# Kernel optimization log

Measured on AMD Instinct MI355X. Metric: run time of the kernel, lower is better.

## Reference

```python
import jax, jax.numpy as jnp
import numpy as np


def squash(s):
    # s: (..., d); v = ||s|| / (1 + ||s||^2) * s
    norm = jnp.linalg.norm(s, axis=-1, keepdims=True)
    return norm / (1.0 + norm * norm) * s


def setup_inputs() -> dict:
    key = jax.random.key(0)
    k1, k2, k3 = jax.random.split(key, 3)
    batch, n_in, d_in, n_out, d_out = 256, 1152, 8, 10, 16
    u_i = jax.random.normal(k1, (batch, n_in, d_in), dtype=jnp.float32)
    weight = jax.random.normal(k2, (1, n_in, n_out, d_in, d_out), dtype=jnp.float32)
    bias = jax.random.normal(k3, (n_in, n_out, 1), dtype=jnp.float32)
    return {"u_i": u_i, "weight": weight, "bias": bias, "r": 3}


def reference(u_i, weight, bias, r):
    batch, n_in, d_in = u_i.shape
    # predictions u_j|i: (batch, n_in, n_out, d_out)
    u_ji = jnp.einsum('bnd,node->bnoe', u_i, weight[0]) + bias  # bias (n_in,n_out,1) broadcasts over d_out
    # dynamic routing
    b = jnp.zeros(u_ji.shape[:3], dtype=u_ji.dtype)  # (batch, n_in, n_out)
    v = None
    for _ in range(r):  # r is a small static iteration count
        c = jax.nn.softmax(b, axis=-1)                      # over n_out
        s = jnp.einsum('bno,bnoe->boe', c, u_ji)            # weighted sum over n_in
        v = squash(s)                                       # (batch, n_out, d_out)
        b = b + jnp.einsum('bnoe,boe->bno', u_ji, v)        # agreement update
    return v
```

## Files before the change

### kernel.cpp

```cpp
#include <hip/hip_runtime.h>


#define B    256
#define N    1152
#define NO   10
#define DI   8
#define DE   16
#define NTILE   8
#define NTILES  144
#define BG      64
#define BGS     4
#define THREADS 320
#define KT      (NTILE * DI)

#define SP_OFF 0
#define SP_SZ  (NTILES * B * NO * DE)
#define VS_OFF (SP_OFF + SP_SZ)
#define VS_SZ  (B * NO * DE)

__global__ __launch_bounds__(THREADS, 3)
void routing_kernel(const float* __restrict__ u,
                    const float* __restrict__ w,
                    const float* __restrict__ bias,
                    const float* __restrict__ vsum,
                    float* __restrict__ s_part,
                    const int has_v) {
    __shared__ float lds_u[KT * BG];
    __shared__ float lgx[2][NO][BG];
    const int tid  = threadIdx.x;
    const int lane = tid & 63;
    const int wv   = __builtin_amdgcn_readfirstlane(tid >> 6);
    const int o0   = wv * 2;
    const int b0   = blockIdx.y * BG;
    const int b    = b0 + lane;
    const int n0   = blockIdx.x * NTILE;

    for (int i = tid; i < BG * (KT / 4); i += THREADS) {
        const int r  = i >> 4;
        const int c4 = i & 15;
        const float4 v4 = *((const float4*)u + (size_t)(b0 + r) * (N * DI / 4)
                            + n0 * (DI / 4) + c4);
        const int k = c4 * 4;
        lds_u[(k + 0) * BG + r] = v4.x;
        lds_u[(k + 1) * BG + r] = v4.y;
        lds_u[(k + 2) * BG + r] = v4.z;
        lds_u[(k + 3) * BG + r] = v4.w;
    }

    float4 vv[2][4];
#pragma unroll
    for (int oi = 0; oi < 2; ++oi)
#pragma unroll
        for (int eq = 0; eq < 4; ++eq)
            vv[oi][eq] = make_float4(0.f, 0.f, 0.f, 0.f);
    if (has_v) {
#pragma unroll
        for (int oi = 0; oi < 2; ++oi)
#pragma unroll
            for (int eq = 0; eq < 4; ++eq)
                vv[oi][eq] = *(const float4*)(vsum + ((size_t)b * NO + o0 + oi) * DE + eq * 4);
    }

    float4 acc[2][4];
#pragma unroll
    for (int oi = 0; oi < 2; ++oi)
#pragma unroll
        for (int eq = 0; eq < 4; ++eq)
            acc[oi][eq] = make_float4(0.f, 0.f, 0.f, 0.f);

    __syncthreads();

    for (int i = 0; i < NTILE; ++i) {
        const int n = n0 + i;

        float ur[DI];
#pragma unroll
        for (int d = 0; d < DI; ++d) ur[d] = lds_u[(i * DI + d) * BG + lane];

        const float* wp = w + ((size_t)n * NO + o0) * (DI * DE);
        float4 uji[2][4];
#pragma unroll
        for (int oi = 0; oi < 2; ++oi) {
            const float bv = bias[n * NO + o0 + oi];
#pragma unroll
            for (int eq = 0; eq < 4; ++eq)
                uji[oi][eq] = make_float4(bv, bv, bv, bv);
#pragma unroll
            for (int d = 0; d < DI; ++d) {
                const float* wrow = wp + oi * (DI * DE) + d * DE;
#pragma unroll
                for (int eq = 0; eq < 4; ++eq) {
                    const float4 w4 = *(const float4*)(wrow + eq * 4);
                    uji[oi][eq].x += ur[d] * w4.x;
                    uji[oi][eq].y += ur[d] * w4.y;
                    uji[oi][eq].z += ur[d] * w4.z;
                    uji[oi][eq].w += ur[d] * w4.w;
                }
            }
        }

        float c[2];
        if (has_v) {
            const int buf = i & 1;
#pragma unroll
            for (int oi = 0; oi < 2; ++oi) {
                float lg = 0.f;
#pragma unroll
                for (int eq = 0; eq < 4; ++eq)
                    lg += uji[oi][eq].x * vv[oi][eq].x + uji[oi][eq].y * vv[oi][eq].y
                        + uji[oi][eq].z * vv[oi][eq].z + uji[oi][eq].w * vv[oi][eq].w;
                lgx[buf][o0 + oi][lane] = lg;
            }
            __syncthreads();
            float l[NO];
#pragma unroll
            for (int o = 0; o < NO; ++o) l[o] = lgx[buf][o][lane];

            float m = l[0];
#pragma unroll
            for (int o = 1; o < NO; ++o) m = fmaxf(m, l[o]);
            float sum = 0.f;
#pragma unroll
            for (int o = 0; o < NO; ++o) { l[o] = __expf(l[o] - m); sum += l[o]; }
            const float inv = 1.f / sum;
            c[0] = l[o0] * inv;
            c[1] = l[o0 + 1] * inv;
        } else {
            c[0] = 0.1f; c[1] = 0.1f;
        }

#pragma unroll
        for (int oi = 0; oi < 2; ++oi)
#pragma unroll
            for (int eq = 0; eq < 4; ++eq) {
                acc[oi][eq].x += c[oi] * uji[oi][eq].x;
                acc[oi][eq].y += c[oi] * uji[oi][eq].y;
                acc[oi][eq].z += c[oi] * uji[oi][eq].z;
                acc[oi][eq].w += c[oi] * uji[oi][eq].w;
            }
    }

    float* sp = s_part + (((size_t)blockIdx.x * B + b) * NO + o0) * DE;
#pragma unroll
    for (int oi = 0; oi < 2; ++oi)
#pragma unroll
        for (int eq = 0; eq < 4; ++eq)
            *(float4*)(sp + oi * DE + eq * 4) = acc[oi][eq];
}

__global__ __launch_bounds__(256)
void squash_kernel(const float* __restrict__ s_part,
                   float* __restrict__ vsum,
                   float* __restrict__ out,
                   const int accum) {
    const int t0 = blockIdx.x * 256 + threadIdx.x;
    const int q  = t0 & 15;
    const int f4 = t0 >> 4;

    const float4* sp = (const float4*)s_part + (size_t)(q * 9) * (B * NO * DE / 4) + f4;
    float4 s = make_float4(0.f, 0.f, 0.f, 0.f);
#pragma unroll
    for (int i = 0; i < 9; ++i) {
        const float4 t = sp[(size_t)i * (B * NO * DE / 4)];
        s.x += t.x; s.y += t.y; s.z += t.z; s.w += t.w;
    }
#pragma unroll
    for (int msk = 1; msk <= 8; msk <<= 1) {
        s.x += __shfl_xor(s.x, msk);
        s.y += __shfl_xor(s.y, msk);
        s.z += __shfl_xor(s.z, msk);
        s.w += __shfl_xor(s.w, msk);
    }
    float nsq = s.x * s.x + s.y * s.y + s.z * s.z + s.w * s.w;
    nsq += __shfl_xor(nsq, 16);
    nsq += __shfl_xor(nsq, 32);
    const float nrm   = sqrtf(nsq);
    const float scale = nrm / (1.f + nsq);

    if (q == 0) {
        const float4 val = make_float4(s.x * scale, s.y * scale, s.z * scale, s.w * scale);
        ((float4*)out)[f4] = val;
        float4* vp = (float4*)vsum + f4;
        if (accum) {
            const float4 old = *vp;
            *vp = make_float4(old.x + val.x, old.y + val.y, old.z + val.z, old.w + val.w);
        } else {
            *vp = val;
        }
    }
}

extern "C" void kernel_launch(void* const* d_in, const int* in_sizes, int n_in,
                              void* d_out, int out_size, void* d_ws, size_t ws_size,
                              hipStream_t stream) {
    const float* u    = (const float*)d_in[0];
    const float* w    = (const float*)d_in[1];
    const float* bias = (const float*)d_in[2];

    float* wsf    = (float*)d_ws;
    float* s_part = wsf + SP_OFF;
    float* vsum   = wsf + VS_OFF;
    float* out    = (float*)d_out;

    for (int it = 0; it < 3; ++it) {
        routing_kernel<<<dim3(NTILES, BGS), THREADS, 0, stream>>>(
            u, w, bias, vsum, s_part, it > 0);
        squash_kernel<<<(16 * B * NO * DE / 4) / 256, 256, 0, stream>>>(
            s_part, vsum, out, it > 0);
    }
}
```

Measured before the change: 212.7 us.

## Stage weight tile in LDS, read u directly, restructure squash reduction

The routing kernel now copies the block's 8-capsule weight tile (40 KB) into LDS and reads each thread's u vector straight from global memory, instead of staging u transposed in LDS and reading weights from global per wave. The squash kernel is also reorganised: each block handles 64 float4 outputs, four waves each sum 36 partials and combine them through LDS, replacing the 16-lane shuffle reduction. This trades global weight traffic for larger LDS use, which may lower occupancy, and the per-thread u loads are strided and uncoalesced.

```diff
diff --git a/kernel.cpp b/kernel.cpp
--- a/kernel.cpp
+++ b/kernel.cpp
@@ -11,7 +11,8 @@
 #define BG      64
 #define BGS     4
 #define THREADS 320
-#define KT      (NTILE * DI)
+#define WFLT    (NO * DI * DE)
+#define WTILE   (NTILE * WFLT)
 
 #define SP_OFF 0
 #define SP_SZ  (NTILES * B * NO * DE)
@@ -25,26 +26,21 @@
                     const float* __restrict__ vsum,
                     float* __restrict__ s_part,
                     const int has_v) {
-    __shared__ float lds_u[KT * BG];
+    __shared__ __align__(16) float lds_w[WTILE];
     __shared__ float lgx[2][NO][BG];
     const int tid  = threadIdx.x;
     const int lane = tid & 63;
     const int wv   = __builtin_amdgcn_readfirstlane(tid >> 6);
     const int o0   = wv * 2;
-    const int b0   = blockIdx.y * BG;
-    const int b    = b0 + lane;
+    const int b    = blockIdx.y * BG + lane;
     const int n0   = blockIdx.x * NTILE;
 
-    for (int i = tid; i < BG * (KT / 4); i += THREADS) {
-        const int r  = i >> 4;
-        const int c4 = i & 15;
-        const float4 v4 = *((const float4*)u + (size_t)(b0 + r) * (N * DI / 4)
-                            + n0 * (DI / 4) + c4);
-        const int k = c4 * 4;
-        lds_u[(k + 0) * BG + r] = v4.x;
-        lds_u[(k + 1) * BG + r] = v4.y;
-        lds_u[(k + 2) * BG + r] = v4.z;
-        lds_u[(k + 3) * BG + r] = v4.w;
+    {
+        const float4* src = (const float4*)(w + (size_t)n0 * WFLT);
+        float4* dst = (float4*)lds_w;
+#pragma unroll
+        for (int j = 0; j < 8; ++j)
+            dst[tid + j * THREADS] = src[tid + j * THREADS];
     }
 
     float4 vv[2][4];
@@ -73,11 +69,12 @@
     for (int i = 0; i < NTILE; ++i) {
         const int n = n0 + i;
 
-        float ur[DI];
-#pragma unroll
-        for (int d = 0; d < DI; ++d) ur[d] = lds_u[(i * DI + d) * BG + lane];
-
-        const float* wp = w + ((size_t)n * NO + o0) * (DI * DE);
+        const float* up = u + ((size_t)b * N + n) * DI;
+        const float4 u0 = *(const float4*)up;
+        const float4 u1 = *(const float4*)(up + 4);
+        const float ur[DI] = {u0.x, u0.y, u0.z, u0.w, u1.x, u1.y, u1.z, u1.w};
+
+        const float* wp = lds_w + i * WFLT + o0 * (DI * DE);
         float4 uji[2][4];
 #pragma unroll
         for (int oi = 0; oi < 2; ++oi) {
@@ -153,37 +150,41 @@
                    float* __restrict__ vsum,
                    float* __restrict__ out,
                    const int accum) {
-    const int t0 = blockIdx.x * 256 + threadIdx.x;
-    const int q  = t0 & 15;
-    const int f4 = t0 >> 4;
-
-    const float4* sp = (const float4*)s_part + (size_t)(q * 9) * (B * NO * DE / 4) + f4;
+    __shared__ __align__(16) float4 part[4][64];
+    const int tid  = threadIdx.x;
+    const int lane = tid & 63;
+    const int q    = tid >> 6;
+    const int f4   = blockIdx.x * 64 + lane;
+
+    const float4* sp = (const float4*)s_part + (size_t)(q * 36) * (B * NO * DE / 4) + f4;
     float4 s = make_float4(0.f, 0.f, 0.f, 0.f);
-#pragma unroll
-    for (int i = 0; i < 9; ++i) {
+#pragma unroll 12
+    for (int i = 0; i < 36; ++i) {
         const float4 t = sp[(size_t)i * (B * NO * DE / 4)];
         s.x += t.x; s.y += t.y; s.z += t.z; s.w += t.w;
     }
-#pragma unroll
-    for (int msk = 1; msk <= 8; msk <<= 1) {
-        s.x += __shfl_xor(s.x, msk);
-        s.y += __shfl_xor(s.y, msk);
-        s.z += __shfl_xor(s.z, msk);
-        s.w += __shfl_xor(s.w, msk);
-    }
-    float nsq = s.x * s.x + s.y * s.y + s.z * s.z + s.w * s.w;
-    nsq += __shfl_xor(nsq, 16);
-    nsq += __shfl_xor(nsq, 32);
-    const float nrm   = sqrtf(nsq);
-    const float scale = nrm / (1.f + nsq);
+    part[q][lane] = s;
+    __syncthreads();
 
     if (q == 0) {
-        const float4 val = make_float4(s.x * scale, s.y * scale, s.z * scale, s.w * scale);
+#pragma unroll
+        for (int j = 1; j < 4; ++j) {
+            const float4 t = part[j][lane];
+            s.x += t.x; s.y += t.y; s.z += t.z; s.w += t.w;
+        }
+        float nsq = s.x * s.x + s.y * s.y + s.z * s.z + s.w * s.w;
+        nsq += __shfl_xor(nsq, 1);
+        nsq += __shfl_xor(nsq, 2);
+        const float nrm   = sqrtf(nsq);
+        const float scale = nrm / (1.f + nsq);
+        const float4 val = make_float4(s.x * scale, s.y * scale,
+                                       s.z * scale, s.w * scale);
         ((float4*)out)[f4] = val;
         float4* vp = (float4*)vsum + f4;
         if (accum) {
             const float4 old = *vp;
-            *vp = make_float4(old.x + val.x, old.y + val.y, old.z + val.z, old.w + val.w);
+            *vp = make_float4(old.x + val.x, old.y + val.y,
+                              old.z + val.z, old.w + val.w);
         } else {
             *vp = val;
         }
@@ -205,7 +206,7 @@
     for (int it = 0; it < 3; ++it) {
         routing_kernel<<<dim3(NTILES, BGS), THREADS, 0, stream>>>(
             u, w, bias, vsum, s_part, it > 0);
-        squash_kernel<<<(16 * B * NO * DE / 4) / 256, 256, 0, stream>>>(
+        squash_kernel<<<(B * NO * DE / 4) / 64, 256, 0, stream>>>(
             s_part, vsum, out, it > 0);
     }
 }
```

Measured after the change: 218.7 us. +2.8%, slower.
